# Kernel optimization log

Measured on AMD Instinct MI355X. Metric: run time of the kernel, lower is better.

The kernel has to match this reference:

```python
import jax, jax.numpy as jnp
import numpy as np

B, N, T = 32, 256, 1024  # batch, num_dimensions, time_dur


def setup_inputs() -> dict:
    key = jax.random.key(0)
    k1, k2 = jax.random.split(key)
    x = jax.random.normal(k1, (B, N, T), dtype=jnp.float32)
    # DBNN.__init__: tau_rise=50, tau_decay=200, omega=2 (all per-dimension)
    tau_rise = jnp.full((N,), 50.0, dtype=jnp.float32)
    tau_decay = jnp.full((N,), 200.0, dtype=jnp.float32)
    omega = jnp.full((N,), 2.0, dtype=jnp.float32)
    # BilinearModified weight: uniform(-1/sqrt(N), 1/sqrt(N)), shape [out=1, N, N]
    bound = 1.0 / np.sqrt(N)
    W = jax.random.uniform(k2, (1, N, N), minval=-bound, maxval=bound, dtype=jnp.float32)
    return {"x": x, "tau_rise": tau_rise, "tau_decay": tau_decay, "omega": omega, "W": W}


def reference(x, tau_rise, tau_decay, omega, W):
    B_, N_, T_ = x.shape
    BIAS = -70.0  # fixed bias buffer in BilinearModified

    # --- create_kernels: [N, T] exponential rise/decay kernels ---
    t = jnp.arange(T_, dtype=x.dtype)
    kernels = (omega[:, None]
               * (1.0 - jnp.exp(-t / tau_rise[:, None]))
               * jnp.exp(-t / tau_decay[:, None]))  # [N, T]

    # torch flips the kernel then runs cross-correlation (conv1d) => causal convolution
    k_flipped = jnp.flip(kernels, axis=-1)[:, None, :]  # [N, 1, T] (OIW, depthwise)

    y = jax.lax.conv_general_dilated(
        x, k_flipped,
        window_strides=(1,),
        padding=[(T_ - 1, T_ - 1)],
        dimension_numbers=("NCH", "OIH", "NCH"),
        feature_group_count=N_,
    )[:, :, :T_]  # [B, N, T]

    yt = jnp.transpose(y, (0, 2, 1))  # [B, T, N]

    # Bilinear with diagonal of weight zeroed (mask-multiply, equivalent to the
    # in-place diagonal-zeroing loop in the torch module)
    Wm = W * (1.0 - jnp.eye(N_, dtype=W.dtype))  # [1, N, N]
    bilinear = jnp.einsum("btn,onm,btm->bto", yt, Wm, yt)  # [B, T, 1]

    linear = jnp.sum(yt, axis=2, keepdims=True)  # [B, T, 1]
    out = bilinear + BIAS + linear
    return out[..., 0]  # [B, T]
```

## Files before the change

### kernel.cpp

```cpp
#include <hip/hip_runtime.h>

typedef _Float16 f16;
typedef _Float16 f16x8 __attribute__((ext_vector_type(8)));
typedef float    f32x4 __attribute__((ext_vector_type(4)));

#define NB 32
#define ND 256
#define NT 1024

__global__ __launch_bounds__(256) void iir_scan_kernel(
    const float* __restrict__ x, const float* __restrict__ tau_rise,
    const float* __restrict__ tau_decay, const float* __restrict__ omega,
    f16* __restrict__ y16)
{
    const int lane = threadIdx.x & 63;
    const int wid  = threadIdx.x >> 6;
    const int row  = blockIdx.x * 4 + wid;
    const int n    = row & (ND - 1);

    const float td = tau_decay[n];
    const float tr = tau_rise[n];
    const float om = omega[n];
    const float ad = expf(-1.0f / td);
    const float am = expf(-(1.0f / tr + 1.0f / td));

    const float* xr = x + (size_t)row * NT + lane * 16;
    float xv[16];
    #pragma unroll
    for (int i = 0; i < 4; ++i) {
        f32x4 v = *reinterpret_cast<const f32x4*>(xr + i * 4);
        xv[i*4+0] = v[0]; xv[i*4+1] = v[1]; xv[i*4+2] = v[2]; xv[i*4+3] = v[3];
    }

    float ld[16], lm[16];
    float sd = 0.f, sm = 0.f;
    #pragma unroll
    for (int i = 0; i < 16; ++i) {
        sd = fmaf(ad, sd, xv[i]); ld[i] = sd;
        sm = fmaf(am, sm, xv[i]); lm[i] = sm;
    }

    float t2;
    t2 = ad * ad; t2 = t2 * t2; t2 = t2 * t2; const float a16d = t2 * t2;
    t2 = am * am; t2 = t2 * t2; t2 = t2 * t2; const float a16m = t2 * t2;

    float Xd = sd, Xm = sm;
    float wdp = a16d, wmp = a16m;
    #pragma unroll
    for (int off = 1; off < 64; off <<= 1) {
        float pd = __shfl_up(Xd, off);
        float pm = __shfl_up(Xm, off);
        if (lane >= off) { Xd = fmaf(wdp, pd, Xd); Xm = fmaf(wmp, pm, Xm); }
        wdp *= wdp; wmp *= wmp;
    }
    float cd = __shfl_up(Xd, 1);
    float cm = __shfl_up(Xm, 1);
    if (lane == 0) { cd = 0.f; cm = 0.f; }

    f16x8 o0, o1;
    float pd = ad, pm = am;
    #pragma unroll
    for (int i = 0; i < 16; ++i) {
        float yd = fmaf(pd, cd, ld[i]);
        float ym = fmaf(pm, cm, lm[i]);
        float yv = om * (yd - ym);
        if (i < 8) o0[i] = (f16)yv; else o1[i - 8] = (f16)yv;
        pd *= ad; pm *= am;
    }
    f16* dst = y16 + (size_t)row * NT + lane * 16;
    *reinterpret_cast<f16x8*>(dst)     = o0;
    *reinterpret_cast<f16x8*>(dst + 8) = o1;
}

__global__ __launch_bounds__(256) void wprep_kernel(
    const float* __restrict__ W, f16* __restrict__ wf)
{
    const int gid  = blockIdx.x * 256 + threadIdx.x;
    const int nh   = gid >> 12;
    const int rem  = gid & 4095;
    const int ks   = rem >> 9;
    const int nt   = (rem >> 6) & 7;
    const int lane = rem & 63;
    const int nrow = nh * 128 + nt * 16 + (lane & 15);
    const int m0   = ks * 32 + (lane >> 4) * 8;
    f16x8 v;
    #pragma unroll
    for (int j = 0; j < 8; ++j) {
        int m = m0 + j;
        float w = W[nrow * 256 + m];
        v[j] = (f16)((m == nrow) ? 0.0f : w);
    }
    *reinterpret_cast<f16x8*>(wf + (size_t)gid * 8) = v;
}

__global__ __launch_bounds__(512, 1) void bilinear_kernel(
    const f16* __restrict__ y16, const f16* __restrict__ wf,
    float* __restrict__ out)
{
    __shared__ __align__(16) f16 Wl[32768];
    __shared__ __align__(16) f16 Yl[32768];

    const int bi = blockIdx.x;
    const int tt = bi & 7;
    const int b  = bi >> 3;
    const int t0 = tt * 128;
    const int tid = threadIdx.x;

    {
        const int m    = tid & 255;
        const int half = tid >> 8;
        const f16* ysrc = y16 + ((size_t)(b * ND + m)) * NT + t0 + half * 64;
        #pragma unroll
        for (int c = 0; c < 8; ++c) {
            f16x8 v = *reinterpret_cast<const f16x8*>(ysrc + c * 8);
            #pragma unroll
            for (int e = 0; e < 8; ++e) {
                int tl = half * 64 + c * 8 + e;
                Yl[tl * 256 + (m ^ (e << 3))] = v[e];
            }
        }
    }

    const int lane = tid & 63;
    const int w    = tid >> 6;
    const int tl   = w * 16 + (lane & 15);
    const int g    = lane >> 4;
    const int sw   = (tl & 7) << 3;

    float part = 0.f;

    #pragma unroll
    for (int nh = 0; nh < 2; ++nh) {
        __syncthreads();
        const f16* wsrc = wf + (size_t)nh * 32768;
        #pragma unroll
        for (int k = 0; k < 8; ++k) {
            int chunk = k * 512 + tid;
            *reinterpret_cast<f16x8*>(&Wl[chunk * 8]) =
                *reinterpret_cast<const f16x8*>(&wsrc[(size_t)chunk * 8]);
        }
        __syncthreads();

        f32x4 acc[8];
        #pragma unroll
        for (int i = 0; i < 8; ++i) acc[i] = (f32x4){0.f, 0.f, 0.f, 0.f};

        #pragma unroll
        for (int ks = 0; ks < 8; ++ks) {
            const int k0 = ks * 32 + g * 8;
            f16x8 bfrag = *reinterpret_cast<const f16x8*>(&Yl[tl * 256 + (k0 ^ sw)]);
            #pragma unroll
            for (int nt = 0; nt < 8; ++nt) {
                f16x8 afrag = *reinterpret_cast<const f16x8*>(
                    &Wl[((ks * 8 + nt) * 64 + lane) * 8]);
                acc[nt] = __builtin_amdgcn_mfma_f32_16x16x32_f16(
                    afrag, bfrag, acc[nt], 0, 0, 0);
            }
        }

        #pragma unroll
        for (int nt = 0; nt < 8; ++nt) {
            #pragma unroll
            for (int r = 0; r < 4; ++r) {
                int ng = nh * 128 + nt * 16 + g * 4 + r;
                float yv = (float)Yl[tl * 256 + (ng ^ sw)];
                part = fmaf(yv, acc[nt][r] + 1.0f, part);
            }
        }
    }

    part += __shfl_xor(part, 16);
    part += __shfl_xor(part, 32);
    if (lane < 16) {
        out[b * NT + t0 + w * 16 + lane] = part - 70.0f;
    }
}

extern "C" void kernel_launch(void* const* d_in, const int* in_sizes, int n_in,
                              void* d_out, int out_size, void* d_ws, size_t ws_size,
                              hipStream_t stream) {
    const float* x         = (const float*)d_in[0];
    const float* tau_rise  = (const float*)d_in[1];
    const float* tau_decay = (const float*)d_in[2];
    const float* omega     = (const float*)d_in[3];
    const float* W         = (const float*)d_in[4];
    float* out = (float*)d_out;

    f16* y16 = (f16*)d_ws;
    f16* wfr = (f16*)((char*)d_ws + (size_t)16 * 1024 * 1024);

    wprep_kernel<<<32, 256, 0, stream>>>(W, wfr);
    iir_scan_kernel<<<(NB * ND) / 4, 256, 0, stream>>>(x, tau_rise, tau_decay, omega, y16);
    bilinear_kernel<<<NB * 8, 512, 0, stream>>>(y16, wfr, out);
}
```

Before: 28.73 us.

## Fuse weight prep into IIR kernel and retile bilinear MFMA for register reuse

Merges the weight-preparation kernel into the IIR scan launch as extra blocks, removing one kernel launch. The bilinear kernel is retiled so each wave computes a 4x4 block of MFMA tiles (4 n-tiles by 4 t-tiles) over the whole K range, reusing A and B fragments across MFMAs instead of reloading Y fragments per n-tile. It also prefetches both W halves and the Y data into registers before writing shared memory, so the second W half's global load overlaps with compute. Per-wave partial sums are combined through a small shared buffer, at the cost of more accumulator registers and an extra barrier.

```diff
diff --git a/kernel.cpp b/kernel.cpp
--- a/kernel.cpp
+++ b/kernel.cpp
@@ -1,6 +1,7 @@
 #include <hip/hip_runtime.h>
 
 typedef _Float16 f16;
+typedef _Float16 f16x4 __attribute__((ext_vector_type(4)));
 typedef _Float16 f16x8 __attribute__((ext_vector_type(8)));
 typedef float    f32x4 __attribute__((ext_vector_type(4)));
 
@@ -8,11 +9,30 @@
 #define ND 256
 #define NT 1024
 
-__global__ __launch_bounds__(256) void iir_scan_kernel(
+__global__ __launch_bounds__(256) void iir_wprep_kernel(
     const float* __restrict__ x, const float* __restrict__ tau_rise,
     const float* __restrict__ tau_decay, const float* __restrict__ omega,
-    f16* __restrict__ y16)
+    const float* __restrict__ W, f16* __restrict__ y16, f16* __restrict__ wf)
 {
+    if (blockIdx.x >= 2048) {
+        const int gid  = (blockIdx.x - 2048) * 256 + threadIdx.x;
+        const int kh   = gid >> 12;
+        const int ks   = (gid >> 10) & 3;
+        const int nt   = (gid >> 6) & 15;
+        const int lane = gid & 63;
+        const int nrow = nt * 16 + (lane & 15);
+        const int k0   = kh * 128 + ks * 32 + (lane >> 4) * 8;
+        f16x8 v;
+        #pragma unroll
+        for (int j = 0; j < 8; ++j) {
+            int k = k0 + j;
+            float w = W[nrow * 256 + k];
+            v[j] = (f16)((k == nrow) ? 0.0f : w);
+        }
+        *reinterpret_cast<f16x8*>(wf + (size_t)gid * 8) = v;
+        return;
+    }
+
     const int lane = threadIdx.x & 63;
     const int wid  = threadIdx.x >> 6;
     const int row  = blockIdx.x * 4 + wid;
@@ -72,33 +92,13 @@
     *reinterpret_cast<f16x8*>(dst + 8) = o1;
 }
 
-__global__ __launch_bounds__(256) void wprep_kernel(
-    const float* __restrict__ W, f16* __restrict__ wf)
-{
-    const int gid  = blockIdx.x * 256 + threadIdx.x;
-    const int nh   = gid >> 12;
-    const int rem  = gid & 4095;
-    const int ks   = rem >> 9;
-    const int nt   = (rem >> 6) & 7;
-    const int lane = rem & 63;
-    const int nrow = nh * 128 + nt * 16 + (lane & 15);
-    const int m0   = ks * 32 + (lane >> 4) * 8;
-    f16x8 v;
-    #pragma unroll
-    for (int j = 0; j < 8; ++j) {
-        int m = m0 + j;
-        float w = W[nrow * 256 + m];
-        v[j] = (f16)((m == nrow) ? 0.0f : w);
-    }
-    *reinterpret_cast<f16x8*>(wf + (size_t)gid * 8) = v;
-}
-
 __global__ __launch_bounds__(512, 1) void bilinear_kernel(
     const f16* __restrict__ y16, const f16* __restrict__ wf,
     float* __restrict__ out)
 {
     __shared__ __align__(16) f16 Wl[32768];
     __shared__ __align__(16) f16 Yl[32768];
+    __shared__ float sbuf[4][128];
 
     const int bi = blockIdx.x;
     const int tt = bi & 7;
@@ -106,73 +106,105 @@
     const int t0 = tt * 128;
     const int tid = threadIdx.x;
 
-    {
-        const int m    = tid & 255;
-        const int half = tid >> 8;
-        const f16* ysrc = y16 + ((size_t)(b * ND + m)) * NT + t0 + half * 64;
-        #pragma unroll
-        for (int c = 0; c < 8; ++c) {
-            f16x8 v = *reinterpret_cast<const f16x8*>(ysrc + c * 8);
-            #pragma unroll
-            for (int e = 0; e < 8; ++e) {
-                int tl = half * 64 + c * 8 + e;
-                Yl[tl * 256 + (m ^ (e << 3))] = v[e];
-            }
-        }
-    }
+    const int m    = tid & 255;
+    const int half = tid >> 8;
+    const f16* ysrc = y16 + ((size_t)(b * ND + m)) * NT + t0 + half * 64;
+    f16x8 vy[8];
+    #pragma unroll
+    for (int c = 0; c < 8; ++c)
+        vy[c] = *reinterpret_cast<const f16x8*>(ysrc + c * 8);
+
+    f16x8 vw[8];
+    #pragma unroll
+    for (int k = 0; k < 8; ++k)
+        vw[k] = *reinterpret_cast<const f16x8*>(&wf[(size_t)(k * 512 + tid) * 8]);
+
+    #pragma unroll
+    for (int c = 0; c < 8; ++c) {
+        #pragma unroll
+        for (int e = 0; e < 8; ++e) {
+            int tl = half * 64 + c * 8 + e;
+            Yl[tl * 256 + (m ^ (e << 3))] = vy[c][e];
+        }
+    }
+    #pragma unroll
+    for (int k = 0; k < 8; ++k)
+        *reinterpret_cast<f16x8*>(&Wl[(k * 512 + tid) * 8]) = vw[k];
+    #pragma unroll
+    for (int k = 0; k < 8; ++k)
+        vw[k] = *reinterpret_cast<const f16x8*>(
+            &wf[(size_t)(32768 / 8 + k * 512 + tid) * 8]);
 
     const int lane = tid & 63;
     const int w    = tid >> 6;
-    const int tl   = w * 16 + (lane & 15);
+    const int wt   = w >> 2;
+    const int wn   = w & 3;
     const int g    = lane >> 4;
-    const int sw   = (tl & 7) << 3;
-
-    float part = 0.f;
-
-    #pragma unroll
-    for (int nh = 0; nh < 2; ++nh) {
+
+    int tl4[4], sw4[4];
+    #pragma unroll
+    for (int tf = 0; tf < 4; ++tf) {
+        tl4[tf] = wt * 64 + tf * 16 + (lane & 15);
+        sw4[tf] = (tl4[tf] & 7) << 3;
+    }
+
+    f32x4 acc[4][4];
+    #pragma unroll
+    for (int a = 0; a < 4; ++a)
+        #pragma unroll
+        for (int tf = 0; tf < 4; ++tf) acc[a][tf] = (f32x4){0.f,0.f,0.f,0.f};
+
+    #pragma unroll
+    for (int kh = 0; kh < 2; ++kh) {
         __syncthreads();
-        const f16* wsrc = wf + (size_t)nh * 32768;
-        #pragma unroll
-        for (int k = 0; k < 8; ++k) {
-            int chunk = k * 512 + tid;
-            *reinterpret_cast<f16x8*>(&Wl[chunk * 8]) =
-                *reinterpret_cast<const f16x8*>(&wsrc[(size_t)chunk * 8]);
-        }
-        __syncthreads();
-
-        f32x4 acc[8];
-        #pragma unroll
-        for (int i = 0; i < 8; ++i) acc[i] = (f32x4){0.f, 0.f, 0.f, 0.f};
-
-        #pragma unroll
-        for (int ks = 0; ks < 8; ++ks) {
-            const int k0 = ks * 32 + g * 8;
-            f16x8 bfrag = *reinterpret_cast<const f16x8*>(&Yl[tl * 256 + (k0 ^ sw)]);
-            #pragma unroll
-            for (int nt = 0; nt < 8; ++nt) {
+        if (kh == 1) {
+            #pragma unroll
+            for (int k = 0; k < 8; ++k)
+                *reinterpret_cast<f16x8*>(&Wl[(k * 512 + tid) * 8]) = vw[k];
+            __syncthreads();
+        }
+        #pragma unroll
+        for (int ks = 0; ks < 4; ++ks) {
+            f16x8 bfrag[4];
+            #pragma unroll
+            for (int tf = 0; tf < 4; ++tf) {
+                int m0 = kh * 128 + ks * 32 + g * 8;
+                bfrag[tf] = *reinterpret_cast<const f16x8*>(
+                    &Yl[tl4[tf] * 256 + (m0 ^ sw4[tf])]);
+            }
+            #pragma unroll
+            for (int a = 0; a < 4; ++a) {
+                int nt = wn * 4 + a;
                 f16x8 afrag = *reinterpret_cast<const f16x8*>(
-                    &Wl[((ks * 8 + nt) * 64 + lane) * 8]);
-                acc[nt] = __builtin_amdgcn_mfma_f32_16x16x32_f16(
-                    afrag, bfrag, acc[nt], 0, 0, 0);
+                    &Wl[((ks * 16 + nt) * 64 + lane) * 8]);
+                #pragma unroll
+                for (int tf = 0; tf < 4; ++tf)
+                    acc[a][tf] = __builtin_amdgcn_mfma_f32_16x16x32_f16(
+                        afrag, bfrag[tf], acc[a][tf], 0, 0, 0);
             }
         }
-
-        #pragma unroll
-        for (int nt = 0; nt < 8; ++nt) {
-            #pragma unroll
-            for (int r = 0; r < 4; ++r) {
-                int ng = nh * 128 + nt * 16 + g * 4 + r;
-                float yv = (float)Yl[tl * 256 + (ng ^ sw)];
-                part = fmaf(yv, acc[nt][r] + 1.0f, part);
-            }
-        }
-    }
-
-    part += __shfl_xor(part, 16);
-    part += __shfl_xor(part, 32);
-    if (lane < 16) {
-        out[b * NT + t0 + w * 16 + lane] = part - 70.0f;
+    }
+
+    #pragma unroll
+    for (int tf = 0; tf < 4; ++tf) {
+        float p = 0.f;
+        #pragma unroll
+        for (int a = 0; a < 4; ++a) {
+            int n0 = (wn * 4 + a) * 16 + g * 4;
+            f16x4 yv4 = *reinterpret_cast<const f16x4*>(
+                &Yl[tl4[tf] * 256 + (n0 ^ sw4[tf])]);
+            #pragma unroll
+            for (int r = 0; r < 4; ++r)
+                p = fmaf((float)yv4[r], acc[a][tf][r] + 1.0f, p);
+        }
+        p += __shfl_xor(p, 16);
+        p += __shfl_xor(p, 32);
+        if (lane < 16) sbuf[wn][wt * 64 + tf * 16 + lane] = p;
+    }
+    __syncthreads();
+    if (tid < 128) {
+        out[b * NT + t0 + tid] =
+            sbuf[0][tid] + sbuf[1][tid] + sbuf[2][tid] + sbuf[3][tid] - 70.0f;
     }
 }
 
@@ -189,7 +221,7 @@
     f16* y16 = (f16*)d_ws;
     f16* wfr = (f16*)((char*)d_ws + (size_t)16 * 1024 * 1024);
 
-    wprep_kernel<<<32, 256, 0, stream>>>(W, wfr);
-    iir_scan_kernel<<<(NB * ND) / 4, 256, 0, stream>>>(x, tau_rise, tau_decay, omega, y16);
+    iir_wprep_kernel<<<2048 + 32, 256, 0, stream>>>(
+        x, tau_rise, tau_decay, omega, W, y16, wfr);
     bilinear_kernel<<<NB * 8, 512, 0, stream>>>(y16, wfr, out);
 }
```

Result: faster. 24.37 us (-15.2%).
